# Kernel optimization log

Measured on AMD Instinct MI355X. Metric: run time of the kernel, lower is better.

## Reference

```python
import jax, jax.numpy as jnp
import numpy as np

FEAT = 64
OUT_DIM = 64
INV_SQRT2 = 0.7071067811865476  # Haar cA of a length-1 zero-padded signal is x/sqrt(2)


def setup_inputs() -> dict:
    key = jax.random.key(0)
    k1, k2, k3, k4, k5, k6 = jax.random.split(key, 6)
    batch, node = 4, 8192
    x = jax.random.normal(k1, (batch, node, FEAT), dtype=jnp.float32)
    adj = jax.random.uniform(k2, (node, node), dtype=jnp.float32) / node  # row-normalized-ish dense adjacency
    # per-feature Linear(wave_len=1 -> 1): weight (feat,), bias (feat,)
    nl_w = jax.random.normal(k3, (FEAT,), dtype=jnp.float32)
    nl_b = jax.random.normal(k4, (FEAT,), dtype=jnp.float32) * 0.01
    # linear_out: (out_dim, feat) weight, (out_dim,) bias
    w_out = jax.random.normal(k5, (OUT_DIM, FEAT), dtype=jnp.float32) / np.sqrt(FEAT)
    b_out = jax.random.normal(k6, (OUT_DIM,), dtype=jnp.float32) * 0.01
    return {"x": x, "adj": adj, "nl_w": nl_w, "nl_b": nl_b, "w_out": w_out, "b_out": b_out}


def reference(x, adj, nl_w, nl_b, w_out, b_out):
    # agg[b,i,f] = sum_j adj[i,j] x[b,j,f]
    agg = jnp.einsum('ij,bjf->bif', adj, x)
    # Haar DWT (J=1, zero mode) of each scalar treated as a length-1 signal -> cA = agg/sqrt(2);
    # per-feature Linear(1->1) then acts elementwise across the feature axis.
    agg_nl = agg * (INV_SQRT2 * nl_w) + nl_b  # (batch, node, feat)
    # linear_out over feature dim; dropout is identity in eval mode
    out = jnp.einsum('bnf,of->bno', agg_nl, w_out) + b_out
    return out
```

## Files before the change

### kernel.cpp

```cpp
#include <hip/hip_runtime.h>

#define NODE 8192
#define FEAT 64
#define OUTD 64
#define NCOL 256

typedef float f32x4 __attribute__((ext_vector_type(4)));
typedef short s16x8 __attribute__((ext_vector_type(8)));
typedef short s16x4 __attribute__((ext_vector_type(4)));
typedef int   i32x4 __attribute__((ext_vector_type(4)));

__device__ __forceinline__ short f2bf(float f) {
    unsigned u = __builtin_bit_cast(unsigned, f);
    u += 0x7FFFu + ((u >> 16) & 1u);
    return (short)(u >> 16);
}

__device__ __forceinline__ s16x4 cvt4(const f32x4& v) {
    s16x4 r;
#pragma unroll
    for (int i = 0; i < 4; ++i) r[i] = f2bf(v[i]);
    return r;
}

__global__ void bias2_kernel(const float* __restrict__ nl_b,
                             const float* __restrict__ w_out,
                             const float* __restrict__ b_out,
                             float* __restrict__ bias2) {
    __shared__ float part[4][64];
    const int o = threadIdx.x & 63;
    const int fc = threadIdx.x >> 6;
    float s = 0.f;
#pragma unroll
    for (int i = 0; i < 16; ++i) {
        int f = fc * 16 + i;
        s += nl_b[f] * w_out[o * FEAT + f];
    }
    part[fc][o] = s;
    __syncthreads();
    if (fc == 0)
        bias2[o] = b_out[o] + part[0][o] + part[1][o] + part[2][o] + part[3][o];
}

__global__ __launch_bounds__(256) void init_out_kernel(
    float* __restrict__ out, const float* __restrict__ bias2) {
    const int idx = (int)blockIdx.x * 256 + threadIdx.x;
    f32x4 bv = *(const f32x4*)(bias2 + ((idx & 15) << 2));
    *(f32x4*)(out + (size_t)idx * 4) = bv;
}

__global__ __launch_bounds__(256) void build_ybf_kernel(
    const float* __restrict__ x, const float* __restrict__ nl_w,
    const float* __restrict__ w_out, unsigned short* __restrict__ ybf) {
    __shared__ float xs[64 * 65];
    __shared__ float w2s[64 * 65];
    const int tid = threadIdx.x;
    const int b   = (int)blockIdx.x >> 7;
    const int j0  = ((int)blockIdx.x & 127) << 6;

    const f32x4* src = (const f32x4*)(x + ((size_t)b * NODE + j0) * FEAT);
#pragma unroll
    for (int i = tid; i < 1024; i += 256) {
        f32x4 v = src[i];
        int j = i >> 4, f = (i & 15) << 2;
        float* d = &xs[j * 65 + f];
        d[0] = v[0]; d[1] = v[1]; d[2] = v[2]; d[3] = v[3];
    }
    for (int i = tid; i < 4096; i += 256) {
        int f = i & 63;
        w2s[(i >> 6) * 65 + f] = w_out[i] * (0.70710678118654752f * nl_w[f]);
    }
    __syncthreads();

    const int j  = tid & 63;
    const int o0 = (tid >> 6) << 4;
    float acc[16];
#pragma unroll
    for (int r = 0; r < 16; ++r) acc[r] = 0.f;
    for (int f = 0; f < 64; ++f) {
        float xv = xs[j * 65 + f];
#pragma unroll
        for (int r = 0; r < 16; ++r) acc[r] += w2s[(o0 + r) * 65 + f] * xv;
    }
    const int jn  = j0 + j;
    const int kb  = jn >> 5;
    const int q   = (jn >> 3) & 3;
    const int e   = jn & 7;
    const int c16 = b * 4 + (o0 >> 4);
    unsigned short* dst =
        ybf + ((size_t)(c16 * 256 + kb) * 512) + (size_t)q * 128 + e;
#pragma unroll
    for (int r = 0; r < 16; ++r) dst[r * 8] = (unsigned short)f2bf(acc[r]);
}

__global__ __launch_bounds__(256, 2) void gemm_adj_kernel(
    const float* __restrict__ adj, const unsigned short* __restrict__ ybf,
    float* __restrict__ out) {
    __shared__ __align__(16) unsigned short As[4][4][32 * 40];

    const int tid  = threadIdx.x;
    const int lane = tid & 63;
    const int wv   = tid >> 6;
    const int bi   = (int)blockIdx.x;
    const int rg   = bi >> 3;
    const int cg   = (bi >> 1) & 3;
    const int ks   = bi & 1;
    const int row0 = rg * 128 + wv * 32;
    const int t16  = lane & 15;
    const int quad = lane >> 4;
    const int sr   = lane >> 2;
    const int sc   = lane & 3;

    const float* aGr[2];
    aGr[0] = adj + (size_t)(row0 + sr) * NODE + ks * 4096 + sc * 4;
    aGr[1] = aGr[0] + (size_t)16 * NODE;

    const unsigned short* bpB[4];
#pragma unroll
    for (int nt = 0; nt < 4; ++nt)
        bpB[nt] = ybf + ((size_t)((cg * 4 + nt) * 256 + ks * 128) * 512) + lane * 8;

    unsigned short* Aw = &As[wv][0][0];
    const int woff = sr * 40 + sc * 4;

    f32x4 acc[2][4];
#pragma unroll
    for (int mi = 0; mi < 2; ++mi)
#pragma unroll
        for (int nt = 0; nt < 4; ++nt) acc[mi][nt] = (f32x4){0.f, 0.f, 0.f, 0.f};

    f32x4 aR[4][4];
    i32x4 BF[2][4];

#pragma unroll
    for (int s = 0; s < 4; ++s)
#pragma unroll
        for (int g = 0; g < 2; ++g)
#pragma unroll
            for (int j = 0; j < 2; ++j)
                aR[s][g * 2 + j] = *(const f32x4*)(aGr[g] + s * 32 + j * 16);
#pragma unroll
    for (int nt = 0; nt < 4; ++nt) BF[0][nt] = *(const i32x4*)bpB[nt];
#pragma unroll
    for (int s = 0; s < 2; ++s) {
        unsigned short* wb = Aw + s * 1280;
#pragma unroll
        for (int g = 0; g < 2; ++g)
#pragma unroll
            for (int j = 0; j < 2; ++j)
                *(s16x4*)(wb + g * 640 + j * 16 + woff) = cvt4(aR[s][g * 2 + j]);
#pragma unroll
        for (int g = 0; g < 2; ++g)
#pragma unroll
            for (int j = 0; j < 2; ++j)
                aR[s][g * 2 + j] = *(const f32x4*)(aGr[g] + (4 + s) * 32 + j * 16);
    }

#define ROUND(qv, PH)                                                         \
    {                                                                         \
                                                    \
        const int tB = (qv + 1) & 127;                                        \
        _Pragma("unroll") for (int nt = 0; nt < 4; ++nt)                      \
            BF[(PH + 1) & 1][nt] = *(const i32x4*)(bpB[nt] + (size_t)tB * 512); \
                           \
        {                                                                     \
            unsigned short* wb = Aw + ((PH + 2) & 3) * 1280;                  \
            _Pragma("unroll") for (int g = 0; g < 2; ++g)                     \
                _Pragma("unroll") for (int j = 0; j < 2; ++j)                 \
                    *(s16x4*)(wb + g * 640 + j * 16 + woff) =                 \
                        cvt4(aR[(PH + 2) & 3][g * 2 + j]);                    \
        }                                                                     \
                                 \
        {                                                                     \
            const int ko = ((qv + 6) & 127) * 32;                             \
            _Pragma("unroll") for (int g = 0; g < 2; ++g)                     \
                _Pragma("unroll") for (int j = 0; j < 2; ++j)                 \
                    aR[(PH + 2) & 3][g * 2 + j] =                             \
                        *(const f32x4*)(aGr[g] + ko + j * 16);                \
        }                                                                     \
                                                          \
        {                                                                     \
            const unsigned short* rb = Aw + (PH & 3) * 1280;                  \
            s16x8 af0 = *(const s16x8*)(rb + t16 * 40 + quad * 8);            \
            s16x8 af1 = *(const s16x8*)(rb + (16 + t16) * 40 + quad * 8);     \
            _Pragma("unroll") for (int nt = 0; nt < 4; ++nt) {                \
                s16x8 bf = __builtin_bit_cast(s16x8, BF[PH & 1][nt]);         \
                acc[0][nt] = __builtin_amdgcn_mfma_f32_16x16x32_bf16(         \
                    af0, bf, acc[0][nt], 0, 0, 0);                            \
                acc[1][nt] = __builtin_amdgcn_mfma_f32_16x16x32_bf16(         \
                    af1, bf, acc[1][nt], 0, 0, 0);                            \
            }                                                                 \
        }                                                                     \
    }

#pragma unroll 1
    for (int q = 0; q < 128; q += 4) {
        ROUND(q + 0, 0)
        ROUND(q + 1, 1)
        ROUND(q + 2, 2)
        ROUND(q + 3, 3)
    }
#undef ROUND

#pragma unroll
    for (int mi = 0; mi < 2; ++mi) {
        const int i0 = row0 + mi * 16 + quad * 4;
#pragma unroll
        for (int nt = 0; nt < 4; ++nt) {
            float* op = out + ((size_t)cg * NODE + i0) * OUTD + nt * 16 + t16;
#pragma unroll
            for (int rr = 0; rr < 4; ++rr)
                atomicAdd(op + (size_t)rr * OUTD, acc[mi][nt][rr]);
        }
    }
}

extern "C" void kernel_launch(void* const* d_in, const int* in_sizes, int n_in,
                              void* d_out, int out_size, void* d_ws, size_t ws_size,
                              hipStream_t stream) {
    const float* x     = (const float*)d_in[0];
    const float* adj   = (const float*)d_in[1];
    const float* nl_w  = (const float*)d_in[2];
    const float* nl_b  = (const float*)d_in[3];
    const float* w_out = (const float*)d_in[4];
    const float* b_out = (const float*)d_in[5];
    float* out = (float*)d_out;

    unsigned short* ybf = (unsigned short*)d_ws;
    float* bias2 = (float*)((char*)d_ws + (size_t)NCOL * NODE * 2);

    bias2_kernel<<<1, 256, 0, stream>>>(nl_b, w_out, b_out, bias2);
    init_out_kernel<<<2048, 256, 0, stream>>>(out, bias2);
    build_ybf_kernel<<<512, 256, 0, stream>>>(x, nl_w, w_out, ybf);
    gemm_adj_kernel<<<512, 256, 0, stream>>>(adj, ybf, out);
}
```

Measured before the change: 475.4 us.

## Register-tile ybf build, split GEMM K four ways with XCD-aware block mapping

The ybf build kernel now handles 128 nodes per block and computes a 4x8 register tile per thread from a transposed, padded weight table, writing packed 8-wide bf16 stores instead of scattered 2-byte stores. The adjacency GEMM splits K into four parts instead of two, doubling the grid to 1024 blocks. Block indices are remapped so that consecutive blocks on the same XCD share row groups, which should improve L2 reuse of adj rows and ybf. The cost is twice as many atomicAdd operations into the output.

Result: faster. 455.8 us (-4.1%).

```diff
diff --git a/kernel.cpp b/kernel.cpp
--- a/kernel.cpp
+++ b/kernel.cpp
@@ -52,45 +52,65 @@
 __global__ __launch_bounds__(256) void build_ybf_kernel(
     const float* __restrict__ x, const float* __restrict__ nl_w,
     const float* __restrict__ w_out, unsigned short* __restrict__ ybf) {
-    __shared__ float xs[64 * 65];
-    __shared__ float w2s[64 * 65];
+    __shared__ float xs[128 * 65];
+    __shared__ float w2t[64 * 68];
     const int tid = threadIdx.x;
-    const int b   = (int)blockIdx.x >> 7;
-    const int j0  = ((int)blockIdx.x & 127) << 6;
+    const int b   = (int)blockIdx.x >> 6;
+    const int j0  = ((int)blockIdx.x & 63) << 7;
 
     const f32x4* src = (const f32x4*)(x + ((size_t)b * NODE + j0) * FEAT);
 #pragma unroll
-    for (int i = tid; i < 1024; i += 256) {
+    for (int it = 0; it < 8; ++it) {
+        int i = tid + it * 256;
         f32x4 v = src[i];
-        int j = i >> 4, f = (i & 15) << 2;
-        float* d = &xs[j * 65 + f];
+        int jl = i >> 4, f0 = (i & 15) << 2;
+        float* d = &xs[jl * 65 + f0];
         d[0] = v[0]; d[1] = v[1]; d[2] = v[2]; d[3] = v[3];
     }
-    for (int i = tid; i < 4096; i += 256) {
-        int f = i & 63;
-        w2s[(i >> 6) * 65 + f] = w_out[i] * (0.70710678118654752f * nl_w[f]);
+#pragma unroll
+    for (int it = 0; it < 16; ++it) {
+        int i = tid + it * 256;
+        int o = i >> 6, f = i & 63;
+        w2t[f * 68 + o] = w_out[i] * (0.70710678118654752f * nl_w[f]);
     }
     __syncthreads();
 
-    const int j  = tid & 63;
-    const int o0 = (tid >> 6) << 4;
-    float acc[16];
-#pragma unroll
-    for (int r = 0; r < 16; ++r) acc[r] = 0.f;
+    const int oq = tid & 15;
+    const int J  = tid >> 4;
+    const float* xr = &xs[(J * 8) * 65];
+    const float* wr = &w2t[oq * 4];
+
+    float acc[4][8];
+#pragma unroll
+    for (int i = 0; i < 4; ++i)
+#pragma unroll
+        for (int e = 0; e < 8; ++e) acc[i][e] = 0.f;
+
+#pragma unroll 4
     for (int f = 0; f < 64; ++f) {
-        float xv = xs[j * 65 + f];
-#pragma unroll
-        for (int r = 0; r < 16; ++r) acc[r] += w2s[(o0 + r) * 65 + f] * xv;
-    }
-    const int jn  = j0 + j;
-    const int kb  = jn >> 5;
-    const int q   = (jn >> 3) & 3;
-    const int e   = jn & 7;
-    const int c16 = b * 4 + (o0 >> 4);
-    unsigned short* dst =
-        ybf + ((size_t)(c16 * 256 + kb) * 512) + (size_t)q * 128 + e;
-#pragma unroll
-    for (int r = 0; r < 16; ++r) dst[r * 8] = (unsigned short)f2bf(acc[r]);
+        f32x4 w4 = *(const f32x4*)(wr + f * 68);
+        float xv[8];
+#pragma unroll
+        for (int e = 0; e < 8; ++e) xv[e] = xr[e * 65 + f];
+#pragma unroll
+        for (int i = 0; i < 4; ++i)
+#pragma unroll
+            for (int e = 0; e < 8; ++e) acc[i][e] += w4[i] * xv[e];
+    }
+
+    const int jn0 = j0 + J * 8;
+    const int kb  = jn0 >> 5;
+    const int q   = (jn0 >> 3) & 3;
+    const int c16 = b * 4 + (oq >> 2);
+    unsigned short* dst = ybf + ((size_t)(c16 * 256 + kb) * 512) +
+                          q * 128 + ((oq & 3) * 4) * 8;
+#pragma unroll
+    for (int i = 0; i < 4; ++i) {
+        s16x8 pv;
+#pragma unroll
+        for (int e = 0; e < 8; ++e) pv[e] = f2bf(acc[i][e]);
+        *(s16x8*)(dst + i * 8) = pv;
+    }
 }
 
 __global__ __launch_bounds__(256, 2) void gemm_adj_kernel(
@@ -102,9 +122,11 @@
     const int lane = tid & 63;
     const int wv   = tid >> 6;
     const int bi   = (int)blockIdx.x;
-    const int rg   = bi >> 3;
-    const int cg   = (bi >> 1) & 3;
-    const int ks   = bi & 1;
+    const int xcd  = bi & 7;
+    const int seq  = bi >> 3;
+    const int rg   = (seq >> 4) * 8 + xcd;
+    const int cg   = (seq >> 2) & 3;
+    const int ks   = seq & 3;
     const int row0 = rg * 128 + wv * 32;
     const int t16  = lane & 15;
     const int quad = lane >> 4;
@@ -112,13 +134,13 @@
     const int sc   = lane & 3;
 
     const float* aGr[2];
-    aGr[0] = adj + (size_t)(row0 + sr) * NODE + ks * 4096 + sc * 4;
+    aGr[0] = adj + (size_t)(row0 + sr) * NODE + ks * 2048 + sc * 4;
     aGr[1] = aGr[0] + (size_t)16 * NODE;
 
     const unsigned short* bpB[4];
 #pragma unroll
     for (int nt = 0; nt < 4; ++nt)
-        bpB[nt] = ybf + ((size_t)((cg * 4 + nt) * 256 + ks * 128) * 512) + lane * 8;
+        bpB[nt] = ybf + ((size_t)((cg * 4 + nt) * 256 + ks * 64) * 512) + lane * 8;
 
     unsigned short* Aw = &As[wv][0][0];
     const int woff = sr * 40 + sc * 4;
@@ -159,7 +181,7 @@
 #define ROUND(qv, PH)                                                         \
     {                                                                         \
                                                     \
-        const int tB = (qv + 1) & 127;                                        \
+        const int tB = (qv + 1) & 63;                                         \
         _Pragma("unroll") for (int nt = 0; nt < 4; ++nt)                      \
             BF[(PH + 1) & 1][nt] = *(const i32x4*)(bpB[nt] + (size_t)tB * 512); \
                            \
@@ -172,7 +194,7 @@
         }                                                                     \
                                  \
         {                                                                     \
-            const int ko = ((qv + 6) & 127) * 32;                             \
+            const int ko = ((qv + 6) & 63) * 32;                              \
             _Pragma("unroll") for (int g = 0; g < 2; ++g)                     \
                 _Pragma("unroll") for (int j = 0; j < 2; ++j)                 \
                     aR[(PH + 2) & 3][g * 2 + j] =                             \
@@ -194,7 +216,7 @@
     }
 
 #pragma unroll 1
-    for (int q = 0; q < 128; q += 4) {
+    for (int q = 0; q < 64; q += 4) {
         ROUND(q + 0, 0)
         ROUND(q + 1, 1)
         ROUND(q + 2, 2)
@@ -231,6 +253,6 @@
 
     bias2_kernel<<<1, 256, 0, stream>>>(nl_b, w_out, b_out, bias2);
     init_out_kernel<<<2048, 256, 0, stream>>>(out, bias2);
-    build_ybf_kernel<<<512, 256, 0, stream>>>(x, nl_w, w_out, ybf);
-    gemm_adj_kernel<<<512, 256, 0, stream>>>(adj, ybf, out);
-}
+    build_ybf_kernel<<<256, 256, 0, stream>>>(x, nl_w, w_out, ybf);
+    gemm_adj_kernel<<<1024, 256, 0, stream>>>(adj, ybf, out);
+}
```
